# Optimization experiments

Measured on AMD Instinct MI355X. Metric: run time of the kernel, lower is better.

Reference implementation:

```python
import jax, jax.numpy as jnp
import numpy as np
import math

NP_, NA_ = 100000, 50000          # paper / author node counts
E0, E1, E2 = 300000, 300000, 200000  # author->paper, paper->author, paper->paper
H, D = 4, 16
HID = H * D                       # 64
IN_DIM, OUT_DIM = 128, 64
L = 2                             # num_layers
EPS = 1e-5


def _lin(x, W, b):
    return x @ W + b


def _ln(x, g, b):
    m = jnp.mean(x, axis=-1, keepdims=True)
    v = jnp.mean((x - m) ** 2, axis=-1, keepdims=True)
    return (x - m) * jax.lax.rsqrt(v + EPS) * g + b


def _segment_softmax(a, seg, n):
    m = jax.ops.segment_max(a, seg, num_segments=n)
    a = jnp.exp(a - m[seg])
    s = jax.ops.segment_sum(a, seg, num_segments=n)
    return a / (s[seg] + 1e-16)


def _hgt_conv(h_p, h_a, ei_ap, ei_pa, ei_pp,
              W_kqv, b_kqv, W_krel, W_vrel, p_rel, W_hout, b_hout, skip):
    # per-node-type fused KQV projection (HeteroDictLinear)
    kqv_p = _lin(h_p, W_kqv[0], b_kqv[0])   # [NP, 3*HID]
    kqv_a = _lin(h_a, W_kqv[1], b_kqv[1])   # [NA, 3*HID]
    k_p, q_p, v_p = [t.reshape(-1, H, D) for t in jnp.split(kqv_p, 3, axis=1)]
    k_a, q_a, v_a = [t.reshape(-1, H, D) for t in jnp.split(kqv_a, 3, axis=1)]
    # destination (query) concat order: paper then author -> dst offsets {paper:0, author:NP}
    Q = jnp.concatenate([q_p, q_a], axis=0)                    # [NP+NA, H, D]
    # per-(edge_type, head) DxD relation transforms on source k/v (k_rel / v_rel)
    # src concat order follows edge types: et0 src=author, et1 src=paper, et2 src=paper
    Ks = jnp.concatenate([
        jnp.einsum('nhd,hde->nhe', k_a, W_krel[0]),
        jnp.einsum('nhd,hde->nhe', k_p, W_krel[1]),
        jnp.einsum('nhd,hde->nhe', k_p, W_krel[2]),
    ], axis=0)                                                 # [NA+2*NP, H, D]
    Vs = jnp.concatenate([
        jnp.einsum('nhd,hde->nhe', v_a, W_vrel[0]),
        jnp.einsum('nhd,hde->nhe', v_p, W_vrel[1]),
        jnp.einsum('nhd,hde->nhe', v_p, W_vrel[2]),
    ], axis=0)
    # bipartite global edge index (src offsets: 0, NA, NA+NP; dst offsets: paper 0, author NP)
    src = jnp.concatenate([ei_ap[0], ei_pa[0] + NA_, ei_pp[0] + NA_ + NP_])
    dst = jnp.concatenate([ei_ap[1], ei_pa[1] + NP_, ei_pp[1]])
    p = jnp.concatenate([
        jnp.broadcast_to(p_rel[0], (E0, H)),
        jnp.broadcast_to(p_rel[1], (E1, H)),
        jnp.broadcast_to(p_rel[2], (E2, H)),
    ], axis=0)                                                 # [E, H]
    # edge-wise attention: alpha = (q_i * k_j).sum(-1) * p_rel / sqrt(D), segment-softmax over dst
    alpha = jnp.einsum('ehd,ehd->eh', Q[dst], Ks[src]) * p / math.sqrt(D)
    alpha = _segment_softmax(alpha, dst, NP_ + NA_)
    out = jax.ops.segment_sum(Vs[src] * alpha[:, :, None], dst,
                              num_segments=NP_ + NA_)          # [NP+NA, H, D]
    out = out.reshape(-1, HID)
    g = jax.nn.gelu(out, approximate=False)
    o_p = _lin(g[:NP_], W_hout[0], b_hout[0])
    o_a = _lin(g[NP_:], W_hout[1], b_hout[1])
    a_p = jax.nn.sigmoid(skip[0])
    a_a = jax.nn.sigmoid(skip[1])
    return a_p * o_p + (1.0 - a_p) * h_p, a_a * o_a + (1.0 - a_a) * h_a


def _forward(x_paper, x_author, ei_ap, ei_pa, ei_pp,
             W_in, b_in, W_kqv, b_kqv, W_krel, W_vrel, p_rel,
             W_hout, b_hout, skip, ln_g, ln_b, W_out, b_out):
    h_p = _lin(x_paper, W_in[0], b_in[0])
    h_a = _lin(x_author, W_in[1], b_in[1])
    for l in range(L):
        h_p, h_a = _hgt_conv(h_p, h_a, ei_ap, ei_pa, ei_pp,
                             W_kqv[l], b_kqv[l], W_krel[l], W_vrel[l],
                             p_rel[l], W_hout[l], b_hout[l], skip[l])
        h_p = jax.nn.gelu(_ln(h_p, ln_g[l, 0], ln_b[l, 0]), approximate=False)
        h_a = jax.nn.gelu(_ln(h_a, ln_g[l, 1], ln_b[l, 1]), approximate=False)
        # dropout is identity at eval
    out_p = _lin(h_p, W_out[0], b_out[0])
    out_a = _lin(h_a, W_out[1], b_out[1])
    return jnp.concatenate([out_p, out_a], axis=0)  # [NP+NA, OUT_DIM]


def setup_inputs() -> dict:
    key = jax.random.key(0)
    ks = jax.random.split(key, 20)
    f32 = jnp.float32

    def nrm(k, shape, fan_in):
        return jax.random.normal(k, shape, dtype=f32) * (1.0 / math.sqrt(fan_in))

    inp = {}
    inp['x_paper'] = jax.random.normal(ks[0], (NP_, IN_DIM), dtype=f32)
    inp['x_author'] = jax.random.normal(ks[1], (NA_, IN_DIM), dtype=f32)
    inp['ei_ap'] = jnp.stack([jax.random.randint(ks[2], (E0,), 0, NA_),
                              jax.random.randint(ks[3], (E0,), 0, NP_)]).astype(jnp.int32)
    inp['ei_pa'] = jnp.stack([jax.random.randint(ks[4], (E1,), 0, NP_),
                              jax.random.randint(ks[5], (E1,), 0, NA_)]).astype(jnp.int32)
    inp['ei_pp'] = jnp.stack([jax.random.randint(ks[6], (E2,), 0, NP_),
                              jax.random.randint(ks[7], (E2,), 0, NP_)]).astype(jnp.int32)
    inp['W_in'] = nrm(ks[8], (2, IN_DIM, HID), IN_DIM)
    inp['b_in'] = jnp.zeros((2, HID), f32)
    inp['W_kqv'] = nrm(ks[9], (L, 2, HID, 3 * HID), HID)
    inp['b_kqv'] = jnp.zeros((L, 2, 3 * HID), f32)
    inp['W_krel'] = nrm(ks[10], (L, 3, H, D, D), D)
    inp['W_vrel'] = nrm(ks[11], (L, 3, H, D, D), D)
    inp['p_rel'] = jnp.ones((L, 3, H), f32)
    inp['W_hout'] = nrm(ks[12], (L, 2, HID, HID), HID)
    inp['b_hout'] = jnp.zeros((L, 2, HID), f32)
    inp['skip'] = jnp.ones((L, 2), f32)
    inp['ln_g'] = jnp.ones((L, 2, HID), f32)
    inp['ln_b'] = jnp.zeros((L, 2, HID), f32)
    inp['W_out'] = nrm(ks[13], (2, HID, OUT_DIM), HID)
    inp['b_out'] = jnp.zeros((2, OUT_DIM), f32)
    return inp


def reference(x_paper, x_author, ei_ap, ei_pa, ei_pp,
              W_in, b_in, W_kqv, b_kqv, W_krel, W_vrel, p_rel,
              W_hout, b_hout, skip, ln_g, ln_b, W_out, b_out):
    return _forward(x_paper, x_author, ei_ap, ei_pa, ei_pp,
                    W_in, b_in, W_kqv, b_kqv, W_krel, W_vrel, p_rel,
                    W_hout, b_hout, skip, ln_g, ln_b, W_out, b_out)
```

## Files before the change

### kernel.cpp

```cpp
#include <hip/hip_runtime.h>
#include <hip/hip_bf16.h>

#define NP 100000
#define NA 50000
#define NTOT 150000
#define E0 300000
#define E1 300000
#define E2 200000
#define ETOT 800000
#define NH 4
#define HD 16
#define HID 64
#define IN_DIM 128
#define KQV 192
#define LAYERS 2
#define NSRC 250000
#define JP 320
#define JA 192
#define NCH 586
#define PT 1563
#define AT 782
#define LSPAN 33280

typedef __attribute__((ext_vector_type(8))) short bf16x8;
typedef __attribute__((ext_vector_type(4))) float f32x4;
typedef _Float16 h16x2 __attribute__((ext_vector_type(2)));

__device__ __forceinline__ float gelu_exact(float x) {
    return 0.5f * x * (1.0f + erff(x * 0.7071067811865475f));
}
__device__ __forceinline__ unsigned short f2bf(float f) {
    unsigned u = __float_as_uint(f);
    return (unsigned short)((u + 0x7fffu + ((u >> 16) & 1u)) >> 16);
}
__device__ __forceinline__ float bf2f(unsigned short b) {
    return __uint_as_float((unsigned)b << 16);
}
__device__ __forceinline__ unsigned short f2h(float f) {
    union { _Float16 h; unsigned short u; } c;
    c.h = (_Float16)f;
    return c.u;
}

__device__ __forceinline__ void edge_decode(int e, const int* __restrict__ ei_ap,
                                            const int* __restrict__ ei_pa,
                                            const int* __restrict__ ei_pp,
                                            int& src, int& dst) {
    if (e < E0)            { src = ei_ap[e];                 dst = ei_ap[E0 + e]; }
    else if (e < E0 + E1)  { int le = e - E0;
                             src = NA + ei_pa[le];           dst = NP + ei_pa[E1 + le]; }
    else                   { int le = e - E0 - E1;
                             src = NA + NP + ei_pp[le];      dst = ei_pp[E2 + le]; }
}

__global__ void csr_count_kernel(const int* __restrict__ ei_ap, const int* __restrict__ ei_pa,
                                 const int* __restrict__ ei_pp, int* __restrict__ cnt) {
    int e = blockIdx.x * 256 + threadIdx.x;
    if (e >= ETOT) return;
    int src, dst; edge_decode(e, ei_ap, ei_pa, ei_pp, src, dst);
    atomicAdd(&cnt[dst], 1);
}

__global__ void scan_chunk_sums(const int* __restrict__ cnt, int* __restrict__ csum) {
    __shared__ int sd[256];
    int c = blockIdx.x, t = threadIdx.x;
    int i = c * 256 + t;
    sd[t] = (i < NTOT) ? cnt[i] : 0;
    __syncthreads();
    for (int o = 128; o > 0; o >>= 1) { if (t < o) sd[t] += sd[t + o]; __syncthreads(); }
    if (t == 0) csum[c] = sd[0];
}

__global__ void scan_offsets(const int* __restrict__ csum, int* __restrict__ coff, int nch) {
    __shared__ int sd[1024];
    int t = threadIdx.x;
    int v = (t < nch) ? csum[t] : 0;
    sd[t] = v;
    __syncthreads();
    for (int o = 1; o < 1024; o <<= 1) {
        int x = (t >= o) ? sd[t - o] : 0;
        __syncthreads();
        sd[t] += x;
        __syncthreads();
    }
    if (t < nch) coff[t] = sd[t] - v;
}

__global__ void scan_final(const int* __restrict__ cnt, const int* __restrict__ coff,
                           int* __restrict__ row_ptr, int* __restrict__ cursor) {
    __shared__ int sd[256];
    int c = blockIdx.x, t = threadIdx.x, i = c * 256 + t;
    int v = (i < NTOT) ? cnt[i] : 0;
    sd[t] = v;
    __syncthreads();
    for (int o = 1; o < 256; o <<= 1) {
        int x = (t >= o) ? sd[t - o] : 0;
        __syncthreads();
        sd[t] += x;
        __syncthreads();
    }
    if (i < NTOT) { int ex = coff[c] + sd[t] - v; row_ptr[i] = ex; cursor[i] = ex; }
    if (i == 0) row_ptr[NTOT] = ETOT;
}

__global__ void csr_fill_kernel(const int* __restrict__ ei_ap, const int* __restrict__ ei_pa,
                                const int* __restrict__ ei_pp, int* __restrict__ cursor,
                                int* __restrict__ edge_src) {
    int e = blockIdx.x * 256 + threadIdx.x;
    if (e >= ETOT) return;
    int src, dst; edge_decode(e, ei_ap, ei_pa, ei_pp, src, dst);
    int pos = atomicAdd(&cursor[dst], 1);
    edge_src[pos] = src;
}

__global__ void prep_weights(const float* __restrict__ W_in, const float* __restrict__ W_hout,
                             const float* __restrict__ W_out,
                             unsigned short* __restrict__ WinT,
                             unsigned short* __restrict__ WhoutT,
                             unsigned short* __restrict__ WoutT) {
    int idx = blockIdx.x * 256 + threadIdx.x;
    if (idx < 2 * 64 * IN_DIM) {
        int t = idx >> 13, r = idx & 8191;
        int c = r >> 7, k = r & 127;
        WinT[idx] = f2bf(W_in[(size_t)t * IN_DIM * HID + (size_t)k * HID + c]);
        return;
    }
    int i2 = idx - 2 * 64 * IN_DIM;
    if (i2 < LAYERS * 2 * 4096) {
        int p = i2 >> 12, r = i2 & 4095;
        int c = r >> 6, k = r & 63;
        WhoutT[i2] = f2bf(W_hout[(size_t)p * 4096 + (size_t)k * HID + c]);
        return;
    }
    int i3 = i2 - LAYERS * 2 * 4096;
    if (i3 < 2 * 4096) {
        int p = i3 >> 12, r = i3 & 4095;
        int c = r >> 6, k = r & 63;
        WoutT[i3] = f2bf(W_out[(size_t)p * 4096 + (size_t)k * HID + c]);
    }
}

__global__ void fuse_weights_all(const float* __restrict__ Wkqv, const float* __restrict__ bkqv,
                                 const float* __restrict__ Wkrel, const float* __restrict__ Wvrel,
                                 unsigned short* __restrict__ WfpT, float* __restrict__ bfp,
                                 unsigned short* __restrict__ WfaT, float* __restrict__ bfa) {
    int gidx = blockIdx.x * 256 + threadIdx.x;
    if (gidx >= LAYERS * LSPAN) return;
    int lay = gidx / LSPAN;
    int idx = gidx - lay * LSPAN;
    const float* Wkqv_l = Wkqv + (size_t)lay * 2 * HID * KQV;
    const float* bkqv_l = bkqv + (size_t)lay * 2 * KQV;
    const float* Wkrel_l = Wkrel + (size_t)lay * 3 * NH * HD * HD;
    const float* Wvrel_l = Wvrel + (size_t)lay * 3 * NH * HD * HD;
    unsigned short* WfpT_l = WfpT + (size_t)lay * JP * 64;
    unsigned short* WfaT_l = WfaT + (size_t)lay * JA * 64;
    float* bfp_l = bfp + (size_t)lay * JP;
    float* bfa_l = bfa + (size_t)lay * JA;

    int type, i, j;
    if (idx < 65 * JP) { type = 0; i = idx / JP; j = idx % JP; }
    else {
        int r = idx - 65 * JP;
        type = 1; i = r / JA; j = r % JA;
    }
    int c = j >> 6, jj = j & 63, h = jj >> 4, e = jj & 15;
    const float* Wk = Wkqv_l + (size_t)type * HID * KQV;
    const float* bk = bkqv_l + type * KQV;
    float val;
    if (c == 0) {
        val = (i < 64) ? Wk[i * KQV + 64 + jj] : bk[64 + jj];
    } else {
        int et, isV;
        if (type == 0) { et = (c == 1 || c == 3) ? 1 : 2; isV = (c >= 3); }
        else           { et = 0; isV = (c == 2); }
        const float* Wr = (isV ? Wvrel_l : Wkrel_l) + (size_t)(et * NH + h) * HD * HD;
        int sb = (isV ? 128 : 0) + h * HD;
        val = 0.0f;
        #pragma unroll
        for (int d = 0; d < HD; d++) {
            float a = (i < 64) ? Wk[i * KQV + sb + d] : bk[sb + d];
            val += a * Wr[d * HD + e];
        }
    }
    if (i < 64) (type ? WfaT_l : WfpT_l)[(size_t)j * 64 + i] = f2bf(val);
    else        (type ? bfa_l : bfp_l)[j] = val;
}

__device__ __forceinline__ void mfma64(const unsigned short* A, const unsigned short* W,
                                       int wr, int wc, int lrow, int lgrp,
                                       f32x4& a00, f32x4& a01, f32x4& a10, f32x4& a11) {
    a00 = (f32x4){0.f,0.f,0.f,0.f}; a01 = a00; a10 = a00; a11 = a00;
    #pragma unroll
    for (int ks = 0; ks < 2; ks++) {
        int ko = ks * 32 + lgrp * 8;
        bf16x8 x0 = *(const bf16x8*)&A[(wr + lrow) * 72 + ko];
        bf16x8 x1 = *(const bf16x8*)&A[(wr + 16 + lrow) * 72 + ko];
        bf16x8 w0 = *(const bf16x8*)&W[(wc + lrow) * 72 + ko];
        bf16x8 w1 = *(const bf16x8*)&W[(wc + 16 + lrow) * 72 + ko];
        a00 = __builtin_amdgcn_mfma_f32_16x16x32_bf16(x0, w0, a00, 0, 0, 0);
        a01 = __builtin_amdgcn_mfma_f32_16x16x32_bf16(x0, w1, a01, 0, 0, 0);
        a10 = __builtin_amdgcn_mfma_f32_16x16x32_bf16(x1, w0, a10, 0, 0, 0);
        a11 = __builtin_amdgcn_mfma_f32_16x16x32_bf16(x1, w1, a11, 0, 0, 0);
    }
}

__device__ __forceinline__ void store_q(f32x4 a00, f32x4 a01, f32x4 a10, f32x4 a11,
                                        float bq0, float bq1, int c0, int c1, bool even,
                                        int nb, int N, int wr, int lgrp,
                                        unsigned short* Qbase) {
    #pragma unroll
    for (int mi = 0; mi < 2; mi++) {
        const f32x4 a0 = mi ? a10 : a00;
        const f32x4 a1 = mi ? a11 : a01;
        int rbase = wr + mi * 16 + lgrp * 4;
        #pragma unroll
        for (int r = 0; r < 4; r++) {
            int n = nb + rbase + r;
            unsigned own = (unsigned)f2h(a0[r] + bq0) | ((unsigned)f2h(a1[r] + bq1) << 16);
            unsigned oth = __shfl_xor(own, 1, 64);
            if (even && n < N) {
                unsigned* qp = (unsigned*)(Qbase + (size_t)n * HID);
                qp[c0 >> 1] = (own & 0xffffu) | (oth << 16);
                qp[c1 >> 1] = (own >> 16) | (oth & 0xffff0000u);
            }
        }
    }
}

__device__ __forceinline__ void store_kv(f32x4 k00, f32x4 k01, f32x4 k10, f32x4 k11,
                                         f32x4 v00, f32x4 v01, f32x4 v10, f32x4 v11,
                                         float bk0, float bk1, float bv0, float bv1,
                                         int c0, int c1, bool even,
                                         int nb, int N, int wr, int lgrp,
                                         int noff, unsigned* KVb) {
    #pragma unroll
    for (int mi = 0; mi < 2; mi++) {
        const f32x4 ak0 = mi ? k10 : k00;
        const f32x4 ak1 = mi ? k11 : k01;
        const f32x4 av0 = mi ? v10 : v00;
        const f32x4 av1 = mi ? v11 : v01;
        int rbase = wr + mi * 16 + lgrp * 4;
        #pragma unroll
        for (int r = 0; r < 4; r++) {
            int n = nb + rbase + r;
            unsigned own0 = (unsigned)f2h(ak0[r] + bk0) | ((unsigned)f2h(av0[r] + bv0) << 16);
            unsigned oth0 = __shfl_xor(own0, 1, 64);
            unsigned own1 = (unsigned)f2h(ak1[r] + bk1) | ((unsigned)f2h(av1[r] + bv1) << 16);
            unsigned oth1 = __shfl_xor(own1, 1, 64);
            if (n < N) {
                unsigned* dst = KVb + (((size_t)(noff + n)) << 6);
                unsigned w0 = even ? ((own0 & 0xffffu) | (oth0 << 16))
                                   : ((oth0 >> 16) | (own0 & 0xffff0000u));
                unsigned w1 = even ? ((own1 & 0xffffu) | (oth1 << 16))
                                   : ((oth1 >> 16) | (own1 & 0xffff0000u));
                dst[c0] = w0;
                dst[c1] = w1;
            }
        }
    }
}

__device__ __forceinline__ void kqv_phase(const unsigned short* HS,
                                          unsigned short* PA, unsigned short* PB,
                                          const unsigned short* WT, const float* bias2,
                                          int type, int tid, int nb, int N,
                                          int wr, int wc, int lrow, int lgrp,
                                          int c0, int c1, bool even,
                                          unsigned short* Qh, unsigned* KVb) {
    #pragma unroll
    for (int it = 0; it < 4; it++) {
        int idx = it * 256 + tid;
        int c = idx >> 4, kg = (idx & 15) * 4;
        *(ushort4*)&PA[c * 72 + kg] = *(const ushort4*)(WT + (size_t)c * 64 + kg);
    }
    __syncthreads();
    {
        f32x4 q00, q01, q10, q11;
        mfma64(HS, PA, wr, wc, lrow, lgrp, q00, q01, q10, q11);
        store_q(q00, q01, q10, q11, bias2[c0], bias2[c1], c0, c1, even,
                nb, N, wr, lgrp, Qh + (size_t)(type ? NP : 0) * HID);
    }
    __syncthreads();
    int ng = type ? 1 : 2;
    for (int g = 0; g < ng; g++) {
        int kc = type ? 64 : (g ? 128 : 64);
        int vc = type ? 128 : (g ? 256 : 192);
        int nf = type ? 0 : (g ? NA + NP : NA);
        #pragma unroll
        for (int it = 0; it < 4; it++) {
            int idx = it * 256 + tid;
            int c = idx >> 4, kg = (idx & 15) * 4;
            *(ushort4*)&PA[c * 72 + kg] = *(const ushort4*)(WT + (size_t)(kc + c) * 64 + kg);
            *(ushort4*)&PB[c * 72 + kg] = *(const ushort4*)(WT + (size_t)(vc + c) * 64 + kg);
        }
        __syncthreads();
        f32x4 k00, k01, k10, k11, v00, v01, v10, v11;
        mfma64(HS, PA, wr, wc, lrow, lgrp, k00, k01, k10, k11);
        mfma64(HS, PB, wr, wc, lrow, lgrp, v00, v01, v10, v11);
        store_kv(k00, k01, k10, k11, v00, v01, v10, v11,
                 bias2[kc + c0], bias2[kc + c1], bias2[vc + c0], bias2[vc + c1],
                 c0, c1, even, nb, N, wr, lgrp, nf, KVb);
        __syncthreads();
    }
}

__global__ __launch_bounds__(256) void gemm_in_kqv(
    const float* __restrict__ xp, const float* __restrict__ xa,
    const unsigned short* __restrict__ WinT, const float* __restrict__ b_in,
    const unsigned short* __restrict__ WfpT, const float* __restrict__ bfp,
    const unsigned short* __restrict__ WfaT, const float* __restrict__ bfa,
    unsigned short* __restrict__ Hb, unsigned short* __restrict__ Qh,
    unsigned* __restrict__ KVb)
{
    __shared__ unsigned short smem[17408];
    unsigned short* XB  = smem;
    unsigned short* WTl = smem + 8704;
    unsigned short* HS  = smem;
    unsigned short* PA  = smem + 4608;
    unsigned short* PB  = smem + 9216;

    int b = blockIdx.x, tid = threadIdx.x;
    int type = (b >= PT);
    int tile = type ? (b - PT) : b;
    int N = type ? NA : NP;
    const float* X = type ? xa : xp;
    const unsigned short* WT = WinT + (size_t)type * 64 * IN_DIM;
    const float* bias = b_in + type * HID;
    unsigned short* H = Hb + (type ? (size_t)NP * HID : 0);
    int nb = tile * 64;

    {
        int row = tid >> 2, cg = (tid & 3) * 32;
        int n = nb + row;
        if (n < N) {
            const float* xr = X + (size_t)n * IN_DIM + cg;
            #pragma unroll
            for (int i = 0; i < 32; i += 4) {
                float4 v = *(const float4*)(xr + i);
                *(ushort4*)&XB[row * 136 + cg + i] =
                    make_ushort4(f2bf(v.x), f2bf(v.y), f2bf(v.z), f2bf(v.w));
            }
        } else {
            #pragma unroll
            for (int i = 0; i < 32; i += 4)
                *(ushort4*)&XB[row * 136 + cg + i] = make_ushort4(0, 0, 0, 0);
        }
    }
    #pragma unroll
    for (int it = 0; it < 8; it++) {
        int idx = it * 256 + tid;
        int c = idx >> 5, kg = (idx & 31) * 4;
        *(ushort4*)&WTl[c * 136 + kg] = *(const ushort4*)(WT + (size_t)c * IN_DIM + kg);
    }
    __syncthreads();

    int w = tid >> 6, lane = tid & 63;
    int wr = (w >> 1) * 32, wc = (w & 1) * 32;
    int lrow = lane & 15, lgrp = lane >> 4;
    int c0 = wc + lrow, c1 = wc + 16 + lrow;
    bool even = ((lrow & 1) == 0);

    f32x4 acc00 = {0.f,0.f,0.f,0.f}, acc01 = {0.f,0.f,0.f,0.f};
    f32x4 acc10 = {0.f,0.f,0.f,0.f}, acc11 = {0.f,0.f,0.f,0.f};
    #pragma unroll
    for (int ks = 0; ks < 4; ks++) {
        int ko = ks * 32 + lgrp * 8;
        bf16x8 a0 = *(const bf16x8*)&XB[(wr + lrow) * 136 + ko];
        bf16x8 a1 = *(const bf16x8*)&XB[(wr + 16 + lrow) * 136 + ko];
        bf16x8 b0 = *(const bf16x8*)&WTl[(wc + lrow) * 136 + ko];
        bf16x8 b1 = *(const bf16x8*)&WTl[(wc + 16 + lrow) * 136 + ko];
        acc00 = __builtin_amdgcn_mfma_f32_16x16x32_bf16(a0, b0, acc00, 0, 0, 0);
        acc01 = __builtin_amdgcn_mfma_f32_16x16x32_bf16(a0, b1, acc01, 0, 0, 0);
        acc10 = __builtin_amdgcn_mfma_f32_16x16x32_bf16(a1, b0, acc10, 0, 0, 0);
        acc11 = __builtin_amdgcn_mfma_f32_16x16x32_bf16(a1, b1, acc11, 0, 0, 0);
    }
    __syncthreads();

    float bias0 = bias[c0], bias1 = bias[c1];
    #pragma unroll
    for (int mi = 0; mi < 2; mi++) {
        const f32x4 accn0 = mi ? acc10 : acc00;
        const f32x4 accn1 = mi ? acc11 : acc01;
        int rbase = wr + mi * 16 + lgrp * 4;
        #pragma unroll
        for (int r = 0; r < 4; r++) {
            int n = nb + rbase + r;
            unsigned short h0 = f2bf(accn0[r] + bias0);
            unsigned short h1 = f2bf(accn1[r] + bias1);
            HS[(rbase + r) * 72 + c0] = h0;
            HS[(rbase + r) * 72 + c1] = h1;
            unsigned own = (unsigned)h0 | ((unsigned)h1 << 16);
            unsigned oth = __shfl_xor(own, 1, 64);
            if (even && n < N) {
                unsigned* hp = (unsigned*)(H + (size_t)n * HID);
                hp[c0 >> 1] = (own & 0xffffu) | (oth << 16);
                hp[c1 >> 1] = (own >> 16) | (oth & 0xffff0000u);
            }
        }
    }
    __syncthreads();

    const unsigned short* WT2 = type ? WfaT : WfpT;
    const float* bias2 = type ? bfa : bfp;
    kqv_phase(HS, PA, PB, WT2, bias2, type, tid, nb, N,
              wr, wc, lrow, lgrp, c0, c1, even, Qh, KVb);
}

__global__ __launch_bounds__(256) void attn_kernel(
    const unsigned short* __restrict__ Qh, const unsigned* __restrict__ KVb,
    const float* __restrict__ p_rel, const int* __restrict__ row_ptr,
    const int* __restrict__ edge_src, unsigned short* __restrict__ ABf)
{
    int wid = threadIdx.x >> 6, lane = threadIdx.x & 63;
    int n = blockIdx.x * 4 + wid;
    if (n >= NTOT) return;
    int half = lane >> 5;
    int p = lane & 31;
    int h = p >> 3;
    unsigned qw = *(const unsigned*)(Qh + (((size_t)n) << 6) + 2 * p);
    union { unsigned u; h16x2 v; _Float16 f[2]; } qc; qc.u = qw;
    h16x2 qh = qc.v;
    const float INV_LN2 = 1.4426950408889634f;
    float pr0 = p_rel[h] * 0.25f * INV_LN2;
    float pr1 = p_rel[4 + h] * 0.25f * INV_LN2;
    float pr2 = p_rel[8 + h] * 0.25f * INV_LN2;
    int beg = row_ptr[n], end = row_ptr[n + 1];
    float s = 0.0f, acc0 = 0.f, acc1 = 0.f;
    for (int e = beg; e < end; e += 4) {
        int e0 = e + half;
        int e1 = e + 2 + half;
        bool v0 = (e0 < end), v1 = (e1 < end);
        int s0 = v0 ? edge_src[e0] : 0;
        int s1 = v1 ? edge_src[e1] : 0;
        uint2 kv0 = *(const uint2*)(KVb + (((size_t)s0) << 6) + 2 * p);
        uint2 kv1 = *(const uint2*)(KVb + (((size_t)s1) << 6) + 2 * p);
        float d0, d1;
#if __has_builtin(__builtin_amdgcn_fdot2)
        {
            union { unsigned u; h16x2 v; } ck;
            ck.u = kv0.x; d0 = __builtin_amdgcn_fdot2(qh, ck.v, 0.0f, false);
            ck.u = kv1.x; d1 = __builtin_amdgcn_fdot2(qh, ck.v, 0.0f, false);
        }
#else
        {
            union { unsigned u; _Float16 f[2]; } ck;
            float q0 = (float)qc.f[0], q1 = (float)qc.f[1];
            ck.u = kv0.x; d0 = q0 * (float)ck.f[0] + q1 * (float)ck.f[1];
            ck.u = kv1.x; d1 = q0 * (float)ck.f[0] + q1 * (float)ck.f[1];
        }
#endif
        d0 += __shfl_xor(d0, 1, 64);  d1 += __shfl_xor(d1, 1, 64);
        d0 += __shfl_xor(d0, 2, 64);  d1 += __shfl_xor(d1, 2, 64);
        d0 += __shfl_xor(d0, 4, 64);  d1 += __shfl_xor(d1, 4, 64);
        float pa = (s0 < NA) ? pr0 : ((s0 < NA + NP) ? pr1 : pr2);
        float pb = (s1 < NA) ? pr0 : ((s1 < NA + NP) ? pr1 : pr2);
        float a0 = v0 ? fminf(d0 * pa, 80.0f) : -INFINITY;
        float a1 = v1 ? fminf(d1 * pb, 80.0f) : -INFINITY;
        float p0 = exp2f(a0);
        float p1 = exp2f(a1);
        s += p0 + p1;
        union { unsigned u; _Float16 f[2]; } cv0, cv1;
        cv0.u = kv0.y; cv1.u = kv1.y;
        acc0 += p0 * (float)cv0.f[0] + p1 * (float)cv1.f[0];
        acc1 += p0 * (float)cv0.f[1] + p1 * (float)cv1.f[1];
    }
    s    += __shfl_xor(s, 32, 64);
    acc0 += __shfl_xor(acc0, 32, 64);
    acc1 += __shfl_xor(acc1, 32, 64);
    if (half == 0) {
        float inv = 1.0f / (s + 1e-16f);
        unsigned pack = (unsigned)f2bf(acc0 * inv) | ((unsigned)f2bf(acc1 * inv) << 16);
        *(unsigned*)(ABf + (((size_t)n) << 6) + 2 * p) = pack;
    }
}

__global__ __launch_bounds__(256) void gemm_hout_fused(
    const unsigned short* __restrict__ ABf, const unsigned short* __restrict__ WhT,
    const float* __restrict__ bhout, const float* __restrict__ skip_p,
    const float* __restrict__ lng, const float* __restrict__ lnb,
    unsigned short* __restrict__ Hb,
    const unsigned short* __restrict__ WfpT, const float* __restrict__ bfp,
    const unsigned short* __restrict__ WfaT, const float* __restrict__ bfa,
    unsigned short* __restrict__ Qh, unsigned* __restrict__ KVb,
    const unsigned short* __restrict__ WoT, const float* __restrict__ bout,
    float* __restrict__ outp)
{
    __shared__ unsigned short smem[13824];
    unsigned short* XbS = smem;
    unsigned short* PA  = smem + 4608;
    unsigned short* PB  = smem + 9216;
    float* hs = (float*)(smem + 4608);

    int b = blockIdx.x, tid = threadIdx.x;
    int type = (b >= PT);
    int tile = type ? (b - PT) : b;
    int N = type ? NA : NP;
    size_t base_off = type ? (size_t)NP * HID : 0;
    const unsigned short* X = ABf + base_off;
    const unsigned short* W = WhT + (size_t)type * 4096;
    const float* bias = bhout + type * HID;
    unsigned short* H = Hb + base_off;
    int nb = tile * 64;
    bool fin = (WoT != nullptr);

    {
        int row = tid >> 2, cg = (tid & 3) * 16;
        int n = nb + row;
        unsigned short tmp[16];
        if (n < N) {
            const unsigned short* xr = X + (((size_t)n) << 6) + cg;
            #pragma unroll
            for (int i = 0; i < 16; i += 4) {
                ushort4 v = *(const ushort4*)(xr + i);
                tmp[i]   = f2bf(gelu_exact(bf2f(v.x)));
                tmp[i+1] = f2bf(gelu_exact(bf2f(v.y)));
                tmp[i+2] = f2bf(gelu_exact(bf2f(v.z)));
                tmp[i+3] = f2bf(gelu_exact(bf2f(v.w)));
            }
        } else {
            #pragma unroll
            for (int i = 0; i < 16; i++) tmp[i] = 0;
        }
        #pragma unroll
        for (int i = 0; i < 16; i += 4)
            *(ushort4*)&XbS[row * 72 + cg + i] =
                make_ushort4(tmp[i], tmp[i+1], tmp[i+2], tmp[i+3]);
    }
    #pragma unroll
    for (int it = 0; it < 4; it++) {
        int idx = it * 256 + tid;
        int c = idx >> 4, kg = (idx & 15) * 4;
        *(ushort4*)&PA[c * 72 + kg] = *(const ushort4*)(W + (size_t)c * 64 + kg);
    }
    __syncthreads();

    int w = tid >> 6, lane = tid & 63;
    int wr = (w >> 1) * 32, wc = (w & 1) * 32;
    int lrow = lane & 15, lgrp = lane >> 4;
    int c0 = wc + lrow, c1 = wc + 16 + lrow;
    bool even = ((lrow & 1) == 0);

    f32x4 acc00, acc01, acc10, acc11;
    mfma64(XbS, PA, wr, wc, lrow, lgrp, acc00, acc01, acc10, acc11);
    __syncthreads();

    float a = 1.0f / (1.0f + __expf(-skip_p[type]));
    float oma = 1.0f - a;
    float bias0 = bias[c0], bias1 = bias[c1];
    #pragma unroll
    for (int mi = 0; mi < 2; mi++) {
        const f32x4 accn0 = mi ? acc10 : acc00;
        const f32x4 accn1 = mi ? acc11 : acc01;
        int rbase = wr + mi * 16 + lgrp * 4;
        #pragma unroll
        for (int r = 0; r < 4; r++) {
            int row = rbase + r;
            int n = nb + row;
            if (n < N) {
                const unsigned short* hp = H + (size_t)n * HID;
                hs[row * 68 + c0] = a * (accn0[r] + bias0) + oma * bf2f(hp[c0]);
                hs[row * 68 + c1] = a * (accn1[r] + bias1) + oma * bf2f(hp[c1]);
            } else {
                hs[row * 68 + c0] = 0.f;
                hs[row * 68 + c1] = 0.f;
            }
        }
    }
    __syncthreads();

    const int tr = tid >> 4, tc = tid & 15;
    const int tcj = tc * 4;
    float g0 = lng[type*HID+tcj], g1 = lng[type*HID+tcj+1],
          g2 = lng[type*HID+tcj+2], g3 = lng[type*HID+tcj+3];
    float l0 = lnb[type*HID+tcj], l1 = lnb[type*HID+tcj+1],
          l2 = lnb[type*HID+tcj+2], l3 = lnb[type*HID+tcj+3];
    #pragma unroll 1
    for (int m = 0; m < 4; m++) {
        int row = tr * 4 + m;
        int n = nb + row;
        float v0 = hs[row*68+tcj], v1 = hs[row*68+tcj+1],
              v2 = hs[row*68+tcj+2], v3 = hs[row*68+tcj+3];
        float sum = v0 + v1 + v2 + v3;
        sum += __shfl_xor(sum, 1, 64); sum += __shfl_xor(sum, 2, 64);
        sum += __shfl_xor(sum, 4, 64); sum += __shfl_xor(sum, 8, 64);
        float mean = sum * (1.0f / 64.0f);
        float d0 = v0 - mean, d1 = v1 - mean, d2 = v2 - mean, d3 = v3 - mean;
        float sq = d0*d0 + d1*d1 + d2*d2 + d3*d3;
        sq += __shfl_xor(sq, 1, 64); sq += __shfl_xor(sq, 2, 64);
        sq += __shfl_xor(sq, 4, 64); sq += __shfl_xor(sq, 8, 64);
        float rstd = rsqrtf(sq * (1.0f / 64.0f) + 1e-5f);
        float r0 = gelu_exact(d0 * rstd * g0 + l0);
        float r1 = gelu_exact(d1 * rstd * g1 + l1);
        float r2 = gelu_exact(d2 * rstd * g2 + l2);
        float r3 = gelu_exact(d3 * rstd * g3 + l3);
        hs[row*68+tcj] = r0; hs[row*68+tcj+1] = r1;
        hs[row*68+tcj+2] = r2; hs[row*68+tcj+3] = r3;
        if (!fin && n < N) {
            uint2 pk;
            pk.x = (unsigned)f2bf(r0) | ((unsigned)f2bf(r1) << 16);
            pk.y = (unsigned)f2bf(r2) | ((unsigned)f2bf(r3) << 16);
            *(uint2*)(H + (size_t)n * HID + tcj) = pk;
        }
    }
    __syncthreads();

    {
        int row = tid >> 2, cg = (tid & 3) * 16;
        #pragma unroll
        for (int i = 0; i < 16; i += 4) {
            *(ushort4*)&XbS[row * 72 + cg + i] = make_ushort4(
                f2bf(hs[row*68 + cg + i]),     f2bf(hs[row*68 + cg + i + 1]),
                f2bf(hs[row*68 + cg + i + 2]), f2bf(hs[row*68 + cg + i + 3]));
        }
    }
    __syncthreads();

    if (fin) {
        const unsigned short* W2 = WoT + (size_t)type * 4096;
        #pragma unroll
        for (int it = 0; it < 4; it++) {
            int idx = it * 256 + tid;
            int c = idx >> 4, kg = (idx & 15) * 4;
            *(ushort4*)&PA[c * 72 + kg] = *(const ushort4*)(W2 + (size_t)c * 64 + kg);
        }
        __syncthreads();
        f32x4 o00, o01, o10, o11;
        mfma64(XbS, PA, wr, wc, lrow, lgrp, o00, o01, o10, o11);
        const float* b2 = bout + type * HID;
        float b20 = b2[c0], b21 = b2[c1];
        float* O = outp + base_off;
        #pragma unroll
        for (int mi = 0; mi < 2; mi++) {
            const f32x4 on0 = mi ? o10 : o00;
            const f32x4 on1 = mi ? o11 : o01;
            int rbase = wr + mi * 16 + lgrp * 4;
            #pragma unroll
            for (int r = 0; r < 4; r++) {
                int n = nb + rbase + r;
                if (n >= N) continue;
                O[(size_t)n * HID + c0] = on0[r] + b20;
                O[(size_t)n * HID + c1] = on1[r] + b21;
            }
        }
    } else {
        const unsigned short* WT2 = type ? WfaT : WfpT;
        const float* bias2 = type ? bfa : bfp;
        kqv_phase(XbS, PA, PB, WT2, bias2, type, tid, nb, N,
                  wr, wc, lrow, lgrp, c0, c1, even, Qh, KVb);
    }
}

extern "C" void kernel_launch(void* const* d_in, const int* in_sizes, int n_in,
                              void* d_out, int out_size, void* d_ws, size_t ws_size,
                              hipStream_t stream) {
    const float* x_paper  = (const float*)d_in[0];
    const float* x_author = (const float*)d_in[1];
    const int*   ei_ap    = (const int*)d_in[2];
    const int*   ei_pa    = (const int*)d_in[3];
    const int*   ei_pp    = (const int*)d_in[4];
    const float* W_in     = (const float*)d_in[5];
    const float* b_in     = (const float*)d_in[6];
    const float* W_kqv    = (const float*)d_in[7];
    const float* b_kqv    = (const float*)d_in[8];
    const float* W_krel   = (const float*)d_in[9];
    const float* W_vrel   = (const float*)d_in[10];
    const float* p_rel    = (const float*)d_in[11];
    const float* W_hout   = (const float*)d_in[12];
    const float* b_hout   = (const float*)d_in[13];
    const float* skip     = (const float*)d_in[14];
    const float* ln_g     = (const float*)d_in[15];
    const float* ln_b     = (const float*)d_in[16];
    const float* W_out    = (const float*)d_in[17];
    const float* b_out    = (const float*)d_in[18];
    float* out            = (float*)d_out;

    char* ws = (char*)d_ws;
    unsigned short* Hb  = (unsigned short*)ws;
    unsigned short* Qh  = Hb + (size_t)NTOT * HID;
    unsigned* KVb       = (unsigned*)(Qh + (size_t)NTOT * HID);
    unsigned short* ABf = (unsigned short*)(KVb + (size_t)NSRC * HID);
    unsigned short* WfpT = ABf + (size_t)NTOT * HID;
    float* bfp  = (float*)(WfpT + (size_t)2 * JP * 64);
    unsigned short* WfaT = (unsigned short*)(bfp + 2 * JP);
    float* bfa  = (float*)(WfaT + (size_t)2 * JA * 64);
    unsigned short* WinT   = (unsigned short*)(bfa + 2 * JA);
    unsigned short* WhoutT = WinT + 2 * 64 * IN_DIM;
    unsigned short* WoutT  = WhoutT + LAYERS * 2 * 64 * 64;
    int* cnt      = (int*)(WoutT + 2 * 64 * 64);
    int* row_ptr  = cnt + NTOT;
    int* cursor   = row_ptr + NTOT + 16;
    int* edge_src = cursor + NTOT;
    int* csum     = edge_src + ETOT;
    int* coff     = csum + 1024;

    dim3 blk(256);
    const int EB = (ETOT + 255) / 256;

    hipMemsetAsync(cnt, 0, NTOT * sizeof(int), stream);
    csr_count_kernel<<<EB, blk, 0, stream>>>(ei_ap, ei_pa, ei_pp, cnt);
    scan_chunk_sums<<<NCH, blk, 0, stream>>>(cnt, csum);
    scan_offsets<<<1, 1024, 0, stream>>>(csum, coff, NCH);
    scan_final<<<NCH, blk, 0, stream>>>(cnt, coff, row_ptr, cursor);
    csr_fill_kernel<<<EB, blk, 0, stream>>>(ei_ap, ei_pa, ei_pp, cursor, edge_src);

    prep_weights<<<(2*64*IN_DIM + LAYERS*2*4096 + 2*4096 + 255) / 256, blk, 0, stream>>>(
        W_in, W_hout, W_out, WinT, WhoutT, WoutT);
    fuse_weights_all<<<(LAYERS * LSPAN + 255) / 256, blk, 0, stream>>>(
        W_kqv, b_kqv, W_krel, W_vrel, WfpT, bfp, WfaT, bfa);

    gemm_in_kqv<<<PT + AT, blk, 0, stream>>>(
        x_paper, x_author, WinT, b_in,
        WfpT, bfp, WfaT, bfa, Hb, Qh, KVb);
    attn_kernel<<<(NTOT + 3) / 4, blk, 0, stream>>>(
        Qh, KVb, p_rel, row_ptr, edge_src, ABf);
    gemm_hout_fused<<<PT + AT, blk, 0, stream>>>(
        ABf, WhoutT, b_hout, skip, ln_g, ln_b, Hb,
        WfpT + (size_t)JP * 64, bfp + JP, WfaT + (size_t)JA * 64, bfa + JA,
        Qh, KVb, nullptr, nullptr, nullptr);
    attn_kernel<<<(NTOT + 3) / 4, blk, 0, stream>>>(
        Qh, KVb, p_rel + 3 * NH, row_ptr, edge_src, ABf);
    gemm_hout_fused<<<PT + AT, blk, 0, stream>>>(
        ABf, WhoutT + (size_t)2 * 4096, b_hout + 2 * HID, skip + 2,
        ln_g + 2 * HID, ln_b + 2 * HID, Hb,
        nullptr, nullptr, nullptr, nullptr, Qh, KVb,
        WoutT, b_out, out);
}
```

Before: 349.2 us.

## Keep hout/LayerNorm in registers with row-per-wave MFMA and prefetched weight panels

After: 342.9 us. About the same (-1.8%).

```diff
diff --git a/kernel.cpp b/kernel.cpp
--- a/kernel.cpp
+++ b/kernel.cpp
@@ -303,6 +303,81 @@
         __syncthreads();
     }
 }
+
+__device__ __forceinline__ void mfma_r16(const unsigned short* X, const unsigned short* P,
+                                         int w16, int lrow, int lgrp, f32x4* acc) {
+    #pragma unroll
+    for (int f = 0; f < 4; f++) acc[f] = (f32x4){0.f, 0.f, 0.f, 0.f};
+    #pragma unroll
+    for (int ks = 0; ks < 2; ks++) {
+        int ko = ks * 32 + lgrp * 8;
+        bf16x8 a = *(const bf16x8*)&X[(w16 + lrow) * 72 + ko];
+        #pragma unroll
+        for (int f = 0; f < 4; f++) {
+            bf16x8 bb = *(const bf16x8*)&P[(f * 16 + lrow) * 72 + ko];
+            acc[f] = __builtin_amdgcn_mfma_f32_16x16x32_bf16(a, bb, acc[f], 0, 0, 0);
+        }
+    }
+}
+
+__device__ __forceinline__ void store_q4(const f32x4* q, const float* bias,
+                                         int lrow, int lgrp, int w16, int nb, int N,
+                                         bool even, unsigned short* Qbase) {
+    #pragma unroll
+    for (int fp = 0; fp < 4; fp += 2) {
+        int c0 = fp * 16 + lrow, c1 = c0 + 16;
+        float b0 = bias[c0], b1 = bias[c1];
+        #pragma unroll
+        for (int r = 0; r < 4; r++) {
+            int n = nb + w16 + lgrp * 4 + r;
+            unsigned own = (unsigned)f2h(q[fp][r] + b0) | ((unsigned)f2h(q[fp + 1][r] + b1) << 16);
+            unsigned oth = __shfl_xor(own, 1, 64);
+            if (even && n < N) {
+                unsigned* qp = (unsigned*)(Qbase + (size_t)n * HID);
+                qp[c0 >> 1] = (own & 0xffffu) | (oth << 16);
+                qp[c1 >> 1] = (own >> 16) | (oth & 0xffff0000u);
+            }
+        }
+    }
+}
+
+__device__ __forceinline__ void store_kv4(const f32x4* kk, const f32x4* vv,
+                                          const float* bias, int kc, int vc,
+                                          int lrow, int lgrp, int w16, int nb, int N,
+                                          bool even, int noff, unsigned* KVb) {
+    #pragma unroll
+    for (int fp = 0; fp < 4; fp += 2) {
+        int c0 = fp * 16 + lrow, c1 = c0 + 16;
+        float bk0 = bias[kc + c0], bk1 = bias[kc + c1];
+        float bv0 = bias[vc + c0], bv1 = bias[vc + c1];
+        #pragma unroll
+        for (int r = 0; r < 4; r++) {
+            int n = nb + w16 + lgrp * 4 + r;
+            unsigned own0 = (unsigned)f2h(kk[fp][r] + bk0) | ((unsigned)f2h(vv[fp][r] + bv0) << 16);
+            unsigned oth0 = __shfl_xor(own0, 1, 64);
+            unsigned own1 = (unsigned)f2h(kk[fp + 1][r] + bk1) | ((unsigned)f2h(vv[fp + 1][r] + bv1) << 16);
+            unsigned oth1 = __shfl_xor(own1, 1, 64);
+            if (n < N) {
+                unsigned* dst = KVb + (((size_t)(noff + n)) << 6);
+                unsigned w0 = even ? ((own0 & 0xffffu) | (oth0 << 16))
+                                   : ((oth0 >> 16) | (own0 & 0xffff0000u));
+                unsigned w1 = even ? ((own1 & 0xffffu) | (oth1 << 16))
+                                   : ((oth1 >> 16) | (own1 & 0xffff0000u));
+                dst[c0] = w0;
+                dst[c1] = w1;
+            }
+        }
+    }
+}
+
+#define STAGE_PANEL(dst, src)                                                   \
+    { _Pragma("unroll")                                                         \
+      for (int it_ = 0; it_ < 4; it_++) {                                       \
+          int idx_ = it_ * 256 + tid;                                           \
+          int c_ = idx_ >> 4, kg_ = (idx_ & 15) * 4;                            \
+          *(ushort4*)&dst[c_ * 72 + kg_] =                                      \
+              *(const ushort4*)((src) + (size_t)c_ * 64 + kg_);                 \
+      } }
 
 __global__ __launch_bounds__(256) void gemm_in_kqv(
     const float* __restrict__ xp, const float* __restrict__ xa,
@@ -489,7 +564,6 @@
     unsigned short* XbS = smem;
     unsigned short* PA  = smem + 4608;
     unsigned short* PB  = smem + 9216;
-    float* hs = (float*)(smem + 4608);
 
     int b = blockIdx.x, tid = threadIdx.x;
     int type = (b >= PT);
@@ -526,127 +600,136 @@
             *(ushort4*)&XbS[row * 72 + cg + i] =
                 make_ushort4(tmp[i], tmp[i+1], tmp[i+2], tmp[i+3]);
     }
-    #pragma unroll
-    for (int it = 0; it < 4; it++) {
-        int idx = it * 256 + tid;
-        int c = idx >> 4, kg = (idx & 15) * 4;
-        *(ushort4*)&PA[c * 72 + kg] = *(const ushort4*)(W + (size_t)c * 64 + kg);
-    }
+    STAGE_PANEL(PA, W)
     __syncthreads();
 
     int w = tid >> 6, lane = tid & 63;
-    int wr = (w >> 1) * 32, wc = (w & 1) * 32;
     int lrow = lane & 15, lgrp = lane >> 4;
-    int c0 = wc + lrow, c1 = wc + 16 + lrow;
+    int w16 = w * 16;
     bool even = ((lrow & 1) == 0);
 
-    f32x4 acc00, acc01, acc10, acc11;
-    mfma64(XbS, PA, wr, wc, lrow, lgrp, acc00, acc01, acc10, acc11);
-    __syncthreads();
+    f32x4 acc[4];
+    mfma_r16(XbS, PA, w16, lrow, lgrp, acc);
+    const unsigned short* WT2 = type ? WfaT : WfpT;
+    const float* bias2 = type ? bfa : bfp;
+    STAGE_PANEL(PB, fin ? (WoT + (size_t)type * 4096) : WT2)
 
     float a = 1.0f / (1.0f + __expf(-skip_p[type]));
     float oma = 1.0f - a;
-    float bias0 = bias[c0], bias1 = bias[c1];
-    #pragma unroll
-    for (int mi = 0; mi < 2; mi++) {
-        const f32x4 accn0 = mi ? acc10 : acc00;
-        const f32x4 accn1 = mi ? acc11 : acc01;
-        int rbase = wr + mi * 16 + lgrp * 4;
+    float lnv[4][4];
+    {
+        float bh[4], gg[4], ll[4];
+        #pragma unroll
+        for (int f = 0; f < 4; f++) {
+            int c = f * 16 + lrow;
+            bh[f] = bias[c];
+            gg[f] = lng[type * HID + c];
+            ll[f] = lnb[type * HID + c];
+        }
         #pragma unroll
         for (int r = 0; r < 4; r++) {
-            int row = rbase + r;
-            int n = nb + row;
+            int n = nb + w16 + lgrp * 4 + r;
+            float x0, x1, x2, x3;
             if (n < N) {
                 const unsigned short* hp = H + (size_t)n * HID;
-                hs[row * 68 + c0] = a * (accn0[r] + bias0) + oma * bf2f(hp[c0]);
-                hs[row * 68 + c1] = a * (accn1[r] + bias1) + oma * bf2f(hp[c1]);
-            } else {
-                hs[row * 68 + c0] = 0.f;
-                hs[row * 68 + c1] = 0.f;
+                x0 = a * (acc[0][r] + bh[0]) + oma * bf2f(hp[0 * 16 + lrow]);
+                x1 = a * (acc[1][r] + bh[1]) + oma * bf2f(hp[1 * 16 + lrow]);
+                x2 = a * (acc[2][r] + bh[2]) + oma * bf2f(hp[2 * 16 + lrow]);
+                x3 = a * (acc[3][r] + bh[3]) + oma * bf2f(hp[3 * 16 + lrow]);
+            } else { x0 = x1 = x2 = x3 = 0.f; }
+            float sum = x0 + x1 + x2 + x3;
+            sum += __shfl_xor(sum, 1, 64); sum += __shfl_xor(sum, 2, 64);
+            sum += __shfl_xor(sum, 4, 64); sum += __shfl_xor(sum, 8, 64);
+            float mean = sum * (1.0f / 64.0f);
+            float d0 = x0 - mean, d1 = x1 - mean, d2 = x2 - mean, d3 = x3 - mean;
+            float sq = d0*d0 + d1*d1 + d2*d2 + d3*d3;
+            sq += __shfl_xor(sq, 1, 64); sq += __shfl_xor(sq, 2, 64);
+            sq += __shfl_xor(sq, 4, 64); sq += __shfl_xor(sq, 8, 64);
+            float rstd = rsqrtf(sq * (1.0f / 64.0f) + 1e-5f);
+            lnv[r][0] = gelu_exact(d0 * rstd * gg[0] + ll[0]);
+            lnv[r][1] = gelu_exact(d1 * rstd * gg[1] + ll[1]);
+            lnv[r][2] = gelu_exact(d2 * rstd * gg[2] + ll[2]);
+            lnv[r][3] = gelu_exact(d3 * rstd * gg[3] + ll[3]);
+            if (!fin && n < N) {
+                #pragma unroll
+                for (int fp = 0; fp < 4; fp += 2) {
+                    int c0 = fp * 16 + lrow, c1 = c0 + 16;
+                    unsigned own = (unsigned)f2bf(lnv[r][fp]) | ((unsigned)f2bf(lnv[r][fp + 1]) << 16);
+                    unsigned oth = __shfl_xor(own, 1, 64);
+                    if (even) {
+                        unsigned* hp2 = (unsigned*)(H + (size_t)n * HID);
+                        hp2[c0 >> 1] = (own & 0xffffu) | (oth << 16);
+                        hp2[c1 >> 1] = (own >> 16) | (oth & 0xffff0000u);
+                    }
+                }
+            } else if (!fin) {
+                #pragma unroll
+                for (int fp = 0; fp < 4; fp += 2) {
+                    unsigned own = 0;
+                    (void)__shfl_xor(own, 1, 64);
+                }
             }
         }
     }
     __syncthreads();
 
-    const int tr = tid >> 4, tc = tid & 15;
-    const int tcj = tc * 4;
-    float g0 = lng[type*HID+tcj], g1 = lng[type*HID+tcj+1],
-          g2 = lng[type*HID+tcj+2], g3 = lng[type*HID+tcj+3];
-    float l0 = lnb[type*HID+tcj], l1 = lnb[type*HID+tcj+1],
-          l2 = lnb[type*HID+tcj+2], l3 = lnb[type*HID+tcj+3];
-    #pragma unroll 1
-    for (int m = 0; m < 4; m++) {
-        int row = tr * 4 + m;
-        int n = nb + row;
-        float v0 = hs[row*68+tcj], v1 = hs[row*68+tcj+1],
-              v2 = hs[row*68+tcj+2], v3 = hs[row*68+tcj+3];
-        float sum = v0 + v1 + v2 + v3;
-        sum += __shfl_xor(sum, 1, 64); sum += __shfl_xor(sum, 2, 64);
-        sum += __shfl_xor(sum, 4, 64); sum += __shfl_xor(sum, 8, 64);
-        float mean = sum * (1.0f / 64.0f);
-        float d0 = v0 - mean, d1 = v1 - mean, d2 = v2 - mean, d3 = v3 - mean;
-        float sq = d0*d0 + d1*d1 + d2*d2 + d3*d3;
-        sq += __shfl_xor(sq, 1, 64); sq += __shfl_xor(sq, 2, 64);
-        sq += __shfl_xor(sq, 4, 64); sq += __shfl_xor(sq, 8, 64);
-        float rstd = rsqrtf(sq * (1.0f / 64.0f) + 1e-5f);
-        float r0 = gelu_exact(d0 * rstd * g0 + l0);
-        float r1 = gelu_exact(d1 * rstd * g1 + l1);
-        float r2 = gelu_exact(d2 * rstd * g2 + l2);
-        float r3 = gelu_exact(d3 * rstd * g3 + l3);
-        hs[row*68+tcj] = r0; hs[row*68+tcj+1] = r1;
-        hs[row*68+tcj+2] = r2; hs[row*68+tcj+3] = r3;
-        if (!fin && n < N) {
-            uint2 pk;
-            pk.x = (unsigned)f2bf(r0) | ((unsigned)f2bf(r1) << 16);
-            pk.y = (unsigned)f2bf(r2) | ((unsigned)f2bf(r3) << 16);
-            *(uint2*)(H + (size_t)n * HID + tcj) = pk;
-        }
-    }
-    __syncthreads();
-
-    {
-        int row = tid >> 2, cg = (tid & 3) * 16;
-        #pragma unroll
-        for (int i = 0; i < 16; i += 4) {
-            *(ushort4*)&XbS[row * 72 + cg + i] = make_ushort4(
-                f2bf(hs[row*68 + cg + i]),     f2bf(hs[row*68 + cg + i + 1]),
-                f2bf(hs[row*68 + cg + i + 2]), f2bf(hs[row*68 + cg + i + 3]));
-        }
+    #pragma unroll
+    for (int r = 0; r < 4; r++) {
+        int row = w16 + lgrp * 4 + r;
+        #pragma unroll
+        for (int f = 0; f < 4; f++)
+            XbS[row * 72 + f * 16 + lrow] = f2bf(lnv[r][f]);
     }
     __syncthreads();
 
     if (fin) {
-        const unsigned short* W2 = WoT + (size_t)type * 4096;
-        #pragma unroll
-        for (int it = 0; it < 4; it++) {
-            int idx = it * 256 + tid;
-            int c = idx >> 4, kg = (idx & 15) * 4;
-            *(ushort4*)&PA[c * 72 + kg] = *(const ushort4*)(W2 + (size_t)c * 64 + kg);
-        }
-        __syncthreads();
-        f32x4 o00, o01, o10, o11;
-        mfma64(XbS, PA, wr, wc, lrow, lgrp, o00, o01, o10, o11);
+        f32x4 o[4];
+        mfma_r16(XbS, PB, w16, lrow, lgrp, o);
         const float* b2 = bout + type * HID;
-        float b20 = b2[c0], b21 = b2[c1];
         float* O = outp + base_off;
         #pragma unroll
-        for (int mi = 0; mi < 2; mi++) {
-            const f32x4 on0 = mi ? o10 : o00;
-            const f32x4 on1 = mi ? o11 : o01;
-            int rbase = wr + mi * 16 + lgrp * 4;
+        for (int f = 0; f < 4; f++) {
+            int c = f * 16 + lrow;
+            float bb = b2[c];
             #pragma unroll
             for (int r = 0; r < 4; r++) {
-                int n = nb + rbase + r;
-                if (n >= N) continue;
-                O[(size_t)n * HID + c0] = on0[r] + b20;
-                O[(size_t)n * HID + c1] = on1[r] + b21;
+                int n = nb + w16 + lgrp * 4 + r;
+                if (n < N) O[(size_t)n * HID + c] = o[f][r] + bb;
             }
         }
-    } else {
-        const unsigned short* WT2 = type ? WfaT : WfpT;
-        const float* bias2 = type ? bfa : bfp;
-        kqv_phase(XbS, PA, PB, WT2, bias2, type, tid, nb, N,
-                  wr, wc, lrow, lgrp, c0, c1, even, Qh, KVb);
+        return;
+    }
+
+    int kc1 = 64, vc1 = type ? 128 : 192;
+    int nf1 = type ? 0 : NA;
+    {
+        f32x4 q[4];
+        mfma_r16(XbS, PB, w16, lrow, lgrp, q);
+        STAGE_PANEL(PA, WT2 + (size_t)kc1 * 64)
+        store_q4(q, bias2, lrow, lgrp, w16, nb, N, even,
+                 Qh + (size_t)(type ? NP : 0) * HID);
+    }
+    __syncthreads();
+
+    f32x4 kk[4];
+    mfma_r16(XbS, PA, w16, lrow, lgrp, kk);
+    STAGE_PANEL(PB, WT2 + (size_t)vc1 * 64)
+    __syncthreads();
+
+    {
+        f32x4 vv[4];
+        mfma_r16(XbS, PB, w16, lrow, lgrp, vv);
+        if (type == 0) STAGE_PANEL(PA, WT2 + (size_t)128 * 64)
+        store_kv4(kk, vv, bias2, kc1, vc1, lrow, lgrp, w16, nb, N, even, nf1, KVb);
+    }
+    if (type == 0) {
+        __syncthreads();
+        mfma_r16(XbS, PA, w16, lrow, lgrp, kk);
+        STAGE_PANEL(PB, WT2 + (size_t)256 * 64)
+        __syncthreads();
+        f32x4 vv[4];
+        mfma_r16(XbS, PB, w16, lrow, lgrp, vv);
+        store_kv4(kk, vv, bias2, 128, 256, lrow, lgrp, w16, nb, N, even, NA + NP, KVb);
     }
 }
 
```
